# Kernel optimization log

Measured on AMD Instinct MI355X. Metric: run time of the kernel, lower is better.

The kernel has to match this reference:

```python
import jax, jax.numpy as jnp
import numpy as np

N_DENSE = 13
N_SPARSE = 26
VOCAB = 100000
EMB_DIM = 64
ATTN_HIDDEN = 12
BATCH = 8192
TEMP = 0.1

# pair indices (i < j) over the 26 sparse fields -> 325 pairs
_ROW, _COL = np.triu_indices(N_SPARSE, k=1)


def setup_inputs() -> dict:
    key = jax.random.key(0)
    ks = jax.random.split(key, 10)
    return {
        "dense_x": jax.random.normal(ks[0], (BATCH, N_DENSE), dtype=jnp.float32),
        "sparse_idx": jax.random.randint(ks[1], (BATCH, N_SPARSE), 0, VOCAB, dtype=jnp.int32),
        "emb_tables": jax.random.normal(ks[2], (N_SPARSE, VOCAB, EMB_DIM), dtype=jnp.float32) * 0.01,
        "attn_W": jax.random.normal(ks[3], (EMB_DIM, ATTN_HIDDEN), dtype=jnp.float32) * 0.1,
        "attn_b": jnp.zeros((ATTN_HIDDEN,), dtype=jnp.float32),
        "proj_W": jax.random.normal(ks[4], (ATTN_HIDDEN, 1), dtype=jnp.float32) * 0.1,
        "proj_b": jnp.zeros((1,), dtype=jnp.float32),
        "lin_W": jax.random.normal(ks[5], (N_DENSE + N_SPARSE, 1), dtype=jnp.float32) * 0.01,
        "lin_b": jnp.zeros((1,), dtype=jnp.float32),
        "pred_W": jax.random.normal(ks[6], (EMB_DIM, 1), dtype=jnp.float32) * 0.1,
        "pred_b": jnp.zeros((1,), dtype=jnp.float32),
    }


def reference(dense_x, sparse_idx, emb_tables, attn_W, attn_b, proj_W, proj_b,
              lin_W, lin_b, pred_W, pred_b):
    # linear part operates on the raw concatenated input (sparse ids as floats,
    # exactly as the torch module does via linear_part(x))
    x = jnp.concatenate([dense_x, sparse_idx.astype(jnp.float32)], axis=1)  # [B, 39]
    part_1 = x @ lin_W + lin_b  # [B, 1]

    # per-field embedding gather: [B, 26, D]
    field_ids = jnp.arange(N_SPARSE)[None, :]
    emb = emb_tables[field_ids, sparse_idx]

    # pairwise element-wise cross products: [B, 325, D]
    cross = emb[:, _ROW, :] * emb[:, _COL, :]

    # attention MLP + softmax over pairs (temperature 0.1)
    h = jax.nn.relu(cross @ attn_W + attn_b)            # [B, 325, 12]
    logits = (h @ proj_W + proj_b) / TEMP               # [B, 325, 1]
    scores = jax.nn.softmax(logits, axis=1)

    att_out = jnp.sum(cross * scores, axis=1)           # [B, D]
    part_2 = att_out @ pred_W + pred_b                  # [B, 1]
    return jax.nn.sigmoid(part_1 + part_2)
```

## Files before the change

kernel.cpp:

```cpp
#include <hip/hip_runtime.h>
#include <math.h>

#define N_DENSE  13
#define N_SPARSE 26
#define VOCAB    100000
#define EMB      64
#define NH       12
#define NPAIR    325
#define NTILE    21
#define NPADH    336
#define EBROW    72
#define EBSLOT   2328
#define SSTR     40
#define TEMP_INV 10.0f

typedef __attribute__((ext_vector_type(8))) _Float16 f16x8;
typedef __attribute__((ext_vector_type(4))) float    f32x4;

__device__ __forceinline__ int ebbase(int f) { return f * EBROW + (((f >> 3) & 3) << 3); }

__global__ __launch_bounds__(128, 5) void afm_kernel(
    const float* __restrict__ dense_x,
    const int*   __restrict__ sparse_idx,
    const float* __restrict__ emb,
    const float* __restrict__ attn_W,
    const float* __restrict__ attn_b,
    const float* __restrict__ proj_W,
    const float* __restrict__ proj_b,
    const float* __restrict__ lin_W,
    const float* __restrict__ lin_b,
    const float* __restrict__ pred_W,
    const float* __restrict__ pred_b,
    float* __restrict__ out)
{
    const int tid  = threadIdx.x;
    const int lane = tid & 63;
    const int wv   = tid >> 6;
    const int q    = lane >> 4;
    const int c16  = lane & 15;
    const int row  = __builtin_amdgcn_readfirstlane(blockIdx.x * 2 + wv);

    __shared__ __align__(16) unsigned short eb_s[2][EBSLOT];
    __shared__ __align__(16) unsigned short S_s[2][32 * SSTR];
    __shared__ __align__(16) unsigned short ptab_s[NPADH];

    unsigned short* ebw = &eb_s[wv][0];
    unsigned short* Sb  = &S_s[wv][0];

    const int* sidx = sparse_idx + row * N_SPARSE;
    int myid = (lane < N_SPARSE) ? sidx[lane] : 0;

    float4 vg[7];
    #pragma unroll
    for (int k = 0; k < 7; ++k) {
        int q2  = lane + 64 * k;
        int q2c = q2 < N_SPARSE * 16 ? q2 : N_SPARSE * 16 - 1;
        int f = q2c >> 4, d4 = q2c & 15;
        int idk = __shfl(myid, f);
        vg[k] = *(reinterpret_cast<const float4*>(
                    emb + ((size_t)f * VOCAB + (size_t)idk) * EMB) + d4);
    }

    f16x8 wf[2];
    {
        const bool hok = (c16 < NH);
        const int  hc  = hok ? c16 : 0;
        #pragma unroll
        for (int kt = 0; kt < 2; ++kt) {
            union { f16x8 v; unsigned u32[4]; } u;
            #pragma unroll
            for (int jp = 0; jp < 4; ++jp) {
                int d0 = kt * 32 + q * 8 + jp * 2;
                float w0 = attn_W[d0 * NH + hc];
                float w1 = attn_W[(d0 + 1) * NH + hc];
                if (!hok) { w0 = 0.f; w1 = 0.f; }
                auto hh = __builtin_amdgcn_cvt_pkrtz(w0, w1);
                __builtin_memcpy(&u.u32[jp], &hh, 4);
            }
            wf[kt] = u.v;
        }
    }
    float b4[4], pwh[4];
    #pragma unroll
    for (int r = 0; r < 4; ++r) {
        int h = q * 4 + r;
        bool ok = (h < NH);
        b4[r]  = ok ? attn_b[h] : 0.0f;
        pwh[r] = ok ? proj_W[h] : 0.0f;
    }
    const float pb = proj_b[0];

    {
        const uint4 z = {0u, 0u, 0u, 0u};
        uint4* sb = reinterpret_cast<uint4*>(Sb);
        #pragma unroll
        for (int k2 = 0; k2 < 3; ++k2) {
            int idx = k2 * 64 + lane;
            if (idx < 160) sb[idx] = z;
        }
        uint4* ebq = reinterpret_cast<uint4*>(ebw);
        if (lane < 55) ebq[236 + lane] = z;
    }

    #pragma unroll 1
    for (int p = tid; p < NPADH; p += 128) {
        int pc = p < NPAIR ? p : NPAIR - 1;
        float sf = sqrtf((float)(2601 - 8 * pc));
        int i = (int)((51.0f - sf) * 0.5f);
        int st = (i * (51 - i)) >> 1;
        if (pc < st) { --i; st = (i * (51 - i)) >> 1; }
        else { int st2 = ((i + 1) * (50 - i)) >> 1; if (pc >= st2) { ++i; st = st2; } }
        int j = i + 1 + (pc - st);
        ptab_s[p] = (unsigned short)(i | (j << 8));
    }

    int srcf = lane - N_DENSE;
    int idsh = __shfl(myid, (srcf >= 0 && srcf < N_SPARSE) ? srcf : 0);
    float p1t = 0.0f;
    if (lane < N_DENSE) {
        p1t = dense_x[row * N_DENSE + lane] * lin_W[lane];
    } else if (lane < N_DENSE + N_SPARSE) {
        p1t = (float)idsh * lin_W[lane];
    }

    #pragma unroll
    for (int k = 0; k < 7; ++k) {
        int q2 = lane + 64 * k;
        if (q2 < N_SPARSE * 16) {
            int f = q2 >> 4, d4 = q2 & 15;
            auto h01 = __builtin_amdgcn_cvt_pkrtz(vg[k].x, vg[k].y);
            auto h23 = __builtin_amdgcn_cvt_pkrtz(vg[k].z, vg[k].w);
            uint2 pk;
            __builtin_memcpy(&pk.x, &h01, 4);
            __builtin_memcpy(&pk.y, &h23, 4);
            *reinterpret_cast<uint2*>(&ebw[ebbase(f) + d4 * 4]) = pk;
        }
    }

    __syncthreads();

    float lsum = 0.0f;
    #pragma unroll 3
    for (int t = 0; t < NTILE; ++t) {
        unsigned pt = ptab_s[t * 16 + c16];
        int i = pt & 0xff, j = pt >> 8;

        const f16x8* pi = reinterpret_cast<const f16x8*>(ebw + ebbase(i));
        const f16x8* pj = reinterpret_cast<const f16x8*>(ebw + ebbase(j));
        f16x8 ca = pi[q] * pj[q];
        f16x8 cb = pi[q + 4] * pj[q + 4];

        __builtin_amdgcn_s_setprio(1);
        f32x4 acc = {0.f, 0.f, 0.f, 0.f};
        acc = __builtin_amdgcn_mfma_f32_16x16x32_f16(wf[0], ca, acc, 0, 0, 0);
        acc = __builtin_amdgcn_mfma_f32_16x16x32_f16(wf[1], cb, acc, 0, 0, 0);
        __builtin_amdgcn_s_setprio(0);

        float par =       fmaxf(acc[0] + b4[0], 0.f) * pwh[0];
        par = fmaf(fmaxf(acc[1] + b4[1], 0.f), pwh[1], par);
        par = fmaf(fmaxf(acc[2] + b4[2], 0.f), pwh[2], par);
        par = fmaf(fmaxf(acc[3] + b4[3], 0.f), pwh[3], par);
        par += __shfl_xor(par, 16);
        par += __shfl_xor(par, 32);

        float ev = __expf((par + pb) * TEMP_INV);
        bool valid = (t * 16 + c16) < NPAIR;
        if (q == 0 && valid) {
            _Float16 eh = (_Float16)ev;
            unsigned short hb;
            __builtin_memcpy(&hb, &eh, 2);
            Sb[i * SSTR + j] = hb;
            Sb[j * SSTR + i] = hb;
            lsum += ev;
        }
    }

    #pragma unroll
    for (int o = 32; o > 0; o >>= 1) lsum += __shfl_xor(lsum, o);

    float pw4[4];
    #pragma unroll
    for (int nt = 0; nt < 4; ++nt) pw4[nt] = pred_W[nt * 16 + c16];

    const f16x8 sfr0 = *reinterpret_cast<const f16x8*>(Sb + c16 * SSTR + q * 8);
    const f16x8 sfr1 = *reinterpret_cast<const f16x8*>(Sb + (16 + c16) * SSTR + q * 8);

    float vsum = 0.0f;
    #pragma unroll
    for (int nt = 0; nt < 4; ++nt) {
        const int d = nt * 16 + c16;
        union { f16x8 v; unsigned short u[8]; } bu;
        #pragma unroll
        for (int k = 0; k < 8; ++k)
            bu.u[k] = ebw[584 * q + 72 * k + d];
        __builtin_amdgcn_s_setprio(1);
        f32x4 g0 = {0.f, 0.f, 0.f, 0.f};
        f32x4 g1 = {0.f, 0.f, 0.f, 0.f};
        g0 = __builtin_amdgcn_mfma_f32_16x16x32_f16(sfr0, bu.v, g0, 0, 0, 0);
        g1 = __builtin_amdgcn_mfma_f32_16x16x32_f16(sfr1, bu.v, g1, 0, 0, 0);
        __builtin_amdgcn_s_setprio(0);

        float part = 0.0f;
        #pragma unroll
        for (int r = 0; r < 4; ++r) {
            int i0 = q * 4 + r;
            unsigned short u0 = ebw[ebbase(i0) + d];
            unsigned short u1 = ebw[ebbase(i0 + 16) + d];
            _Float16 h0, h1;
            __builtin_memcpy(&h0, &u0, 2);
            __builtin_memcpy(&h1, &u1, 2);
            part = fmaf((float)h0, g0[r], part);
            part = fmaf((float)h1, g1[r], part);
        }
        vsum = fmaf(part, pw4[nt], vsum);
    }

    float p1 = p1t;
    #pragma unroll
    for (int o = 32; o > 0; o >>= 1) {
        vsum += __shfl_xor(vsum, o);
        p1   += __shfl_xor(p1, o);
    }
    if (lane == 0) {
        float z = p1 + lin_b[0] + 0.5f * vsum / lsum + pred_b[0];
        out[row] = 1.0f / (1.0f + __expf(-z));
    }
}

extern "C" void kernel_launch(void* const* d_in, const int* in_sizes, int n_in,
                              void* d_out, int out_size, void* d_ws, size_t ws_size,
                              hipStream_t stream)
{
    const float* dense_x = (const float*)d_in[0];
    const int*   sparse  = (const int*)  d_in[1];
    const float* emb     = (const float*)d_in[2];
    const float* attn_W  = (const float*)d_in[3];
    const float* attn_b  = (const float*)d_in[4];
    const float* proj_W  = (const float*)d_in[5];
    const float* proj_b  = (const float*)d_in[6];
    const float* lin_W   = (const float*)d_in[7];
    const float* lin_b   = (const float*)d_in[8];
    const float* pred_W  = (const float*)d_in[9];
    const float* pred_b  = (const float*)d_in[10];
    float* out = (float*)d_out;

    int rows = in_sizes[0] / N_DENSE;
    afm_kernel<<<rows / 2, 128, 0, stream>>>(dense_x, sparse, emb, attn_W, attn_b,
                                             proj_W, proj_b, lin_W, lin_b,
                                             pred_W, pred_b, out);
}
```

Before: 34.69 us.

## Fold pred_W projection into attention MFMA as extra output column

Uses the unused 13th column of the attention MFMA weight tile to compute cross·pred_W for each pair, so the weighted sum over pairs becomes a scalar accumulation of exp-score times that projection. This removes the symmetric score matrix in shared memory, its zeroing, the second MFMA stage and the associated LDS traffic, and it also drops the block-wide barrier because each wave now builds its own pair table. The trade-off is that the pred_W projection is computed in fp16 inside the MFMA, and the pair table is redundantly built by both waves.

```diff
diff --git a/kernel.cpp b/kernel.cpp
--- a/kernel.cpp
+++ b/kernel.cpp
@@ -10,8 +10,7 @@
 #define NTILE    21
 #define NPADH    336
 #define EBROW    72
-#define EBSLOT   2328
-#define SSTR     40
+#define EBSLOT   1888
 #define TEMP_INV 10.0f
 
 typedef __attribute__((ext_vector_type(8))) _Float16 f16x8;
@@ -41,11 +40,9 @@
     const int row  = __builtin_amdgcn_readfirstlane(blockIdx.x * 2 + wv);
 
     __shared__ __align__(16) unsigned short eb_s[2][EBSLOT];
-    __shared__ __align__(16) unsigned short S_s[2][32 * SSTR];
     __shared__ __align__(16) unsigned short ptab_s[NPADH];
 
     unsigned short* ebw = &eb_s[wv][0];
-    unsigned short* Sb  = &S_s[wv][0];
 
     const int* sidx = sparse_idx + row * N_SPARSE;
     int myid = (lane < N_SPARSE) ? sidx[lane] : 0;
@@ -63,17 +60,18 @@
 
     f16x8 wf[2];
     {
-        const bool hok = (c16 < NH);
-        const int  hc  = hok ? c16 : 0;
         #pragma unroll
         for (int kt = 0; kt < 2; ++kt) {
             union { f16x8 v; unsigned u32[4]; } u;
             #pragma unroll
             for (int jp = 0; jp < 4; ++jp) {
                 int d0 = kt * 32 + q * 8 + jp * 2;
-                float w0 = attn_W[d0 * NH + hc];
-                float w1 = attn_W[(d0 + 1) * NH + hc];
-                if (!hok) { w0 = 0.f; w1 = 0.f; }
+                float w0, w1;
+                if (c16 < NH)       { w0 = attn_W[d0 * NH + c16];
+                                      w1 = attn_W[(d0 + 1) * NH + c16]; }
+                else if (c16 == NH) { w0 = pred_W[d0];
+                                      w1 = pred_W[d0 + 1]; }
+                else                { w0 = 0.f; w1 = 0.f; }
                 auto hh = __builtin_amdgcn_cvt_pkrtz(w0, w1);
                 __builtin_memcpy(&u.u32[jp], &hh, 4);
             }
@@ -90,20 +88,8 @@
     }
     const float pb = proj_b[0];
 
-    {
-        const uint4 z = {0u, 0u, 0u, 0u};
-        uint4* sb = reinterpret_cast<uint4*>(Sb);
-        #pragma unroll
-        for (int k2 = 0; k2 < 3; ++k2) {
-            int idx = k2 * 64 + lane;
-            if (idx < 160) sb[idx] = z;
-        }
-        uint4* ebq = reinterpret_cast<uint4*>(ebw);
-        if (lane < 55) ebq[236 + lane] = z;
-    }
-
     #pragma unroll 1
-    for (int p = tid; p < NPADH; p += 128) {
+    for (int p = lane; p < NPADH; p += 64) {
         int pc = p < NPAIR ? p : NPAIR - 1;
         float sf = sqrtf((float)(2601 - 8 * pc));
         int i = (int)((51.0f - sf) * 0.5f);
@@ -137,9 +123,7 @@
         }
     }
 
-    __syncthreads();
-
-    float lsum = 0.0f;
+    float lsum = 0.0f, vsum = 0.0f;
     #pragma unroll 3
     for (int t = 0; t < NTILE; ++t) {
         unsigned pt = ptab_s[t * 16 + c16];
@@ -160,69 +144,28 @@
         par = fmaf(fmaxf(acc[1] + b4[1], 0.f), pwh[1], par);
         par = fmaf(fmaxf(acc[2] + b4[2], 0.f), pwh[2], par);
         par = fmaf(fmaxf(acc[3] + b4[3], 0.f), pwh[3], par);
+        float m = (q == 3) ? acc[0] : 0.0f;
+
         par += __shfl_xor(par, 16);
         par += __shfl_xor(par, 32);
+        m   += __shfl_xor(m, 16);
+        m   += __shfl_xor(m, 32);
 
         float ev = __expf((par + pb) * TEMP_INV);
-        bool valid = (t * 16 + c16) < NPAIR;
-        if (q == 0 && valid) {
-            _Float16 eh = (_Float16)ev;
-            unsigned short hb;
-            __builtin_memcpy(&hb, &eh, 2);
-            Sb[i * SSTR + j] = hb;
-            Sb[j * SSTR + i] = hb;
-            lsum += ev;
-        }
-    }
-
-    #pragma unroll
-    for (int o = 32; o > 0; o >>= 1) lsum += __shfl_xor(lsum, o);
-
-    float pw4[4];
-    #pragma unroll
-    for (int nt = 0; nt < 4; ++nt) pw4[nt] = pred_W[nt * 16 + c16];
-
-    const f16x8 sfr0 = *reinterpret_cast<const f16x8*>(Sb + c16 * SSTR + q * 8);
-    const f16x8 sfr1 = *reinterpret_cast<const f16x8*>(Sb + (16 + c16) * SSTR + q * 8);
-
-    float vsum = 0.0f;
-    #pragma unroll
-    for (int nt = 0; nt < 4; ++nt) {
-        const int d = nt * 16 + c16;
-        union { f16x8 v; unsigned short u[8]; } bu;
-        #pragma unroll
-        for (int k = 0; k < 8; ++k)
-            bu.u[k] = ebw[584 * q + 72 * k + d];
-        __builtin_amdgcn_s_setprio(1);
-        f32x4 g0 = {0.f, 0.f, 0.f, 0.f};
-        f32x4 g1 = {0.f, 0.f, 0.f, 0.f};
-        g0 = __builtin_amdgcn_mfma_f32_16x16x32_f16(sfr0, bu.v, g0, 0, 0, 0);
-        g1 = __builtin_amdgcn_mfma_f32_16x16x32_f16(sfr1, bu.v, g1, 0, 0, 0);
-        __builtin_amdgcn_s_setprio(0);
-
-        float part = 0.0f;
-        #pragma unroll
-        for (int r = 0; r < 4; ++r) {
-            int i0 = q * 4 + r;
-            unsigned short u0 = ebw[ebbase(i0) + d];
-            unsigned short u1 = ebw[ebbase(i0 + 16) + d];
-            _Float16 h0, h1;
-            __builtin_memcpy(&h0, &u0, 2);
-            __builtin_memcpy(&h1, &u1, 2);
-            part = fmaf((float)h0, g0[r], part);
-            part = fmaf((float)h1, g1[r], part);
-        }
-        vsum = fmaf(part, pw4[nt], vsum);
+        ev = ((t * 16 + c16) < NPAIR) ? ev : 0.0f;
+        lsum += ev;
+        vsum = fmaf(ev, m, vsum);
     }
 
     float p1 = p1t;
     #pragma unroll
     for (int o = 32; o > 0; o >>= 1) {
+        lsum += __shfl_xor(lsum, o);
         vsum += __shfl_xor(vsum, o);
         p1   += __shfl_xor(p1, o);
     }
     if (lane == 0) {
-        float z = p1 + lin_b[0] + 0.5f * vsum / lsum + pred_b[0];
+        float z = p1 + lin_b[0] + vsum / lsum + pred_b[0];
         out[row] = 1.0f / (1.0f + __expf(-z));
     }
 }
```

Measured after the change: 34.35 us. No clear change (-1.0%).
